# Kernel tuning notes

Hardware: AMD Instinct MI355X
Metric: run time of the kernel (lower is better)

## Reference

```python
import jax, jax.numpy as jnp
import numpy as np

DEPTH = 4
DIM = 1024
HEADS = 16
DIM_HEAD = 64
INNER = HEADS * DIM_HEAD  # 1024
MLP = 4096
CTX = 768
SCALE = DIM_HEAD ** -0.5
EPS = 1e-5


def setup_inputs() -> dict:
    key = jax.random.key(0)
    ks = jax.random.split(key, 12)
    def rn(k, shape, s=0.02):
        return jax.random.normal(k, shape, jnp.float32) * s
    return {
        "x": jax.random.normal(ks[0], (2, 2048, DIM), jnp.float32),
        "context": jax.random.normal(ks[1], (2, 1024, CTX), jnp.float32),
        "ln1_g": jnp.ones((DEPTH, DIM), jnp.float32),
        "ln1_b": jnp.zeros((DEPTH, DIM), jnp.float32),
        "w_qkv": rn(ks[2], (DEPTH, DIM, 3 * INNER)),
        "w_sa_o": rn(ks[3], (DEPTH, INNER, DIM)),
        "b_sa_o": jnp.zeros((DEPTH, DIM), jnp.float32),
        "ln2_g": jnp.ones((DEPTH, DIM), jnp.float32),
        "ln2_b": jnp.zeros((DEPTH, DIM), jnp.float32),
        "w_q": rn(ks[4], (DEPTH, DIM, INNER)),
        "w_kv": rn(ks[5], (DEPTH, CTX, 2 * INNER)),
        "w_ca_o": rn(ks[6], (DEPTH, INNER, DIM)),
        "b_ca_o": jnp.zeros((DEPTH, DIM), jnp.float32),
        "ln3_g": jnp.ones((DEPTH, DIM), jnp.float32),
        "ln3_b": jnp.zeros((DEPTH, DIM), jnp.float32),
        "w_ff1": rn(ks[7], (DEPTH, DIM, MLP)),
        "b_ff1": jnp.zeros((DEPTH, MLP), jnp.float32),
        "w_ff2": rn(ks[8], (DEPTH, MLP, DIM)),
        "b_ff2": jnp.zeros((DEPTH, DIM), jnp.float32),
    }


def _ln(x, g, b):
    mu = jnp.mean(x, axis=-1, keepdims=True)
    var = jnp.mean(jnp.square(x - mu), axis=-1, keepdims=True)
    return (x - mu) * jax.lax.rsqrt(var + EPS) * g + b


def _heads(t):
    # [b, n, h*d] -> [b, h, n, d]
    b, n, _ = t.shape
    return t.reshape(b, n, HEADS, DIM_HEAD).transpose(0, 2, 1, 3)


def _mha(q, k, v):
    # q,k,v: [b, h, n, d]; naive matmul-softmax-matmul, same math as the torch code
    attn = jax.nn.softmax(jnp.einsum('bhqd,bhkd->bhqk', q, k) * SCALE, axis=-1)
    out = jnp.einsum('bhqk,bhkd->bhqd', attn, v)
    b, h, n, d = out.shape
    return out.transpose(0, 2, 1, 3).reshape(b, n, h * d)


def reference(x, context, ln1_g, ln1_b, w_qkv, w_sa_o, b_sa_o,
              ln2_g, ln2_b, w_q, w_kv, w_ca_o, b_ca_o,
              ln3_g, ln3_b, w_ff1, b_ff1, w_ff2, b_ff2):
    for i in range(DEPTH):
        # self-attention
        h = _ln(x, ln1_g[i], ln1_b[i])
        qkv = h @ w_qkv[i]
        q, k, v = jnp.split(qkv, 3, axis=-1)
        sa = _mha(_heads(q), _heads(k), _heads(v)) @ w_sa_o[i] + b_sa_o[i]
        x = sa + x
        # cross-attention
        h = _ln(x, ln2_g[i], ln2_b[i])
        q = h @ w_q[i]
        kv = context @ w_kv[i]
        k, v = jnp.split(kv, 2, axis=-1)
        ca = _mha(_heads(q), _heads(k), _heads(v)) @ w_ca_o[i] + b_ca_o[i]
        x = ca + x
        # feed-forward (exact GELU, matching torch nn.GELU default)
        h = _ln(x, ln3_g[i], ln3_b[i])
        ff = jax.nn.gelu(h @ w_ff1[i] + b_ff1[i], approximate=False) @ w_ff2[i] + b_ff2[i]
        x = ff + x
    return x
```

## Files before the change

kernel.cpp:

```cpp
#include <hip/hip_runtime.h>
#include <hip/hip_bf16.h>
#include <math.h>

typedef __bf16 bf16_t;
typedef __bf16 bf16x8 __attribute__((ext_vector_type(8)));
typedef __bf16 bf16x4 __attribute__((ext_vector_type(4)));
typedef float f32x4 __attribute__((ext_vector_type(4)));
typedef unsigned short u16;
typedef unsigned int u32;
typedef u16 u16x8 __attribute__((ext_vector_type(8)));

#define NDEPTH 4
#define DIM 1024
#define NHEADS 16
#define MLP_DIM 4096
#define CTXD 768
#define NTOK 4096
#define NCTX 2048
#define ATT_SCALE 0.125f

__device__ inline void gload_lds16(const void* g, void* l) {
  __builtin_amdgcn_global_load_lds(
      (const __attribute__((address_space(1))) void*)g,
      (__attribute__((address_space(3))) void*)l, 16, 0, 0);
}

__device__ inline u32 packbf2(float a, float b) {
  union { bf16_t h[2]; u32 w; } u;
  u.h[0] = (bf16_t)a; u.h[1] = (bf16_t)b;
  return u.w;
}

template<int EPI>
__global__ __launch_bounds__(512) void gemm_bf16(
    const bf16_t* __restrict__ A, const bf16_t* __restrict__ Bt,
    const float* __restrict__ bias, const float* __restrict__ res,
    void* __restrict__ outp, int M, int N, int K)
{
  __shared__ alignas(16) bf16_t As[3][128 * 32];
  __shared__ alignas(16) bf16_t Bs[3][128 * 32];
  const int tid = threadIdx.x, lane = tid & 63, wave = tid >> 6;
  const int bx = blockIdx.x, by = blockIdx.y;
  const int wr = wave >> 2, wc = wave & 3;
  const int l15 = lane & 15, l4 = lane >> 4;

  const bf16_t* Ag = A + (size_t)by * 128 * K;
  const bf16_t* Bg = Bt + (size_t)bx * 128 * K;

  f32x4 acc[4][2] = {};

  const int srow = tid >> 2, soff = (tid & 3) * 8;
  auto stage = [&](int buf, int k0) {
    gload_lds16(Ag + (size_t)srow * K + k0 + soff, &As[buf][(size_t)tid * 8]);
    gload_lds16(Bg + (size_t)srow * K + k0 + soff, &Bs[buf][(size_t)tid * 8]);
  };

  const int nk = K >> 5;
  stage(0, 0);
  stage(1, 32);
  asm volatile("s_waitcnt vmcnt(2)" ::: "memory");
  __builtin_amdgcn_s_barrier();
  __builtin_amdgcn_sched_barrier(0);

  for (int t = 0; t < nk; ++t) {
    const int cur = t % 3;
    if (t + 2 < nk) stage((t + 2) % 3, (t + 2) << 5);

    bf16x8 af[4], bfr[2];
#pragma unroll
    for (int mi = 0; mi < 4; ++mi)
      af[mi] = *(const bf16x8*)&As[cur][(wr * 64 + mi * 16 + l15) * 32 + l4 * 8];
#pragma unroll
    for (int ni = 0; ni < 2; ++ni)
      bfr[ni] = *(const bf16x8*)&Bs[cur][(wc * 32 + ni * 16 + l15) * 32 + l4 * 8];
#pragma unroll
    for (int mi = 0; mi < 4; ++mi)
#pragma unroll
      for (int ni = 0; ni < 2; ++ni)
        acc[mi][ni] = __builtin_amdgcn_mfma_f32_16x16x32_bf16(af[mi], bfr[ni], acc[mi][ni], 0, 0, 0);

    if (t + 2 < nk) {
      asm volatile("s_waitcnt vmcnt(2)" ::: "memory");
    } else if (t + 1 < nk) {
      asm volatile("s_waitcnt vmcnt(0)" ::: "memory");
    } else {
      break;
    }
    __builtin_amdgcn_s_barrier();
    __builtin_amdgcn_sched_barrier(0);
  }

  const int r0 = by * 128 + wr * 64, c0 = bx * 128 + wc * 32;
#pragma unroll
  for (int ni = 0; ni < 2; ++ni) {
    int col = c0 + ni * 16 + l15;
    float bv = (EPI == 0) ? 0.f : bias[col];
#pragma unroll
    for (int mi = 0; mi < 4; ++mi) {
#pragma unroll
      for (int r = 0; r < 4; ++r) {
        int row = r0 + mi * 16 + l4 * 4 + r;
        float v = acc[mi][ni][r] + bv;
        size_t idx = (size_t)row * N + col;
        if (EPI == 3) {
          ((float*)outp)[idx] = v + res[idx];
        } else if (EPI == 2) {
          float gv = 0.5f * v * (1.f + erff(v * 0.70710678118f));
          ((bf16_t*)outp)[idx] = (bf16_t)gv;
        } else {
          ((bf16_t*)outp)[idx] = (bf16_t)v;
        }
      }
    }
  }
}

__global__ __launch_bounds__(512) void attn_fwd(
    const bf16_t* __restrict__ Q, int qs,
    const bf16_t* __restrict__ K, const bf16_t* __restrict__ V, int kvs,
    bf16_t* __restrict__ O, int os, int nq, int nk)
{
  __shared__ bf16_t Ks[2][64][72];
  __shared__ bf16_t Vt[2][64][72];

  const int tid = threadIdx.x, lane = tid & 63, wv = tid >> 6;
  const int l15 = lane & 15, l4 = lane >> 4;
  const int h = blockIdx.y, bz = blockIdx.z;
  const size_t qrow0 = (size_t)bz * nq + (size_t)blockIdx.x * 128;
  const bf16_t* Qb = Q + (qrow0 + wv * 16) * qs + h * 64;
  const bf16_t* Kb = K + (size_t)bz * nk * kvs + h * 64;
  const bf16_t* Vb = V + (size_t)bz * nk * kvs + h * 64;
  bf16_t* Ob = O + (qrow0 + wv * 16) * os + h * 64;

  bf16x8 qa[2];
#pragma unroll
  for (int ks = 0; ks < 2; ++ks)
    qa[ks] = *(const bf16x8*)(Qb + (size_t)l15 * qs + ks * 32 + l4 * 8);

  const int krow = tid >> 3, kcol = (tid & 7) * 8;

  u16x8 kreg, vreg;
  auto load_tile = [&](int kt) {
    kreg = *(const u16x8*)(Kb + (size_t)(kt * 64 + krow) * kvs + kcol);
    u16x8 t;
#pragma unroll
    for (int i = 0; i < 8; ++i)
      t[i] = *(const u16*)(Vb + (size_t)(kt * 64 + wv * 8 + i) * kvs + lane);
    vreg = t;
  };
  auto store_tile = [&](int buf) {
    *(u16x8*)&Ks[buf][krow][kcol] = kreg;
    *(u16x8*)&Vt[buf][lane][wv * 8] = vreg;
  };

  float m_run = -1e30f, l_run = 0.f;
  f32x4 acc[4] = {};

  const int ntiles = nk >> 6;
  load_tile(0);
  store_tile(0);
  __syncthreads();

  for (int kt = 0; kt < ntiles; ++kt) {
    const int cur = kt & 1;
    const bool pre = (kt + 1 < ntiles);
    if (pre) load_tile(kt + 1);

    f32x4 s[4] = {};
#pragma unroll
    for (int ks = 0; ks < 2; ++ks)
#pragma unroll
      for (int f = 0; f < 4; ++f) {
        bf16x8 kf = *(const bf16x8*)&Ks[cur][f * 16 + l15][ks * 32 + l4 * 8];
        s[f] = __builtin_amdgcn_mfma_f32_16x16x32_bf16(kf, qa[ks], s[f], 0, 0, 0);
      }

    float smax = s[0][0];
#pragma unroll
    for (int f = 0; f < 4; ++f)
#pragma unroll
      for (int r = 0; r < 4; ++r) smax = fmaxf(smax, s[f][r]);
    smax = fmaxf(smax, __shfl_xor(smax, 16));
    smax = fmaxf(smax, __shfl_xor(smax, 32));
    smax *= ATT_SCALE;
    const float mn = fmaxf(m_run, smax);
    const float esc = __expf(m_run - mn);
    m_run = mn;

    float p[4][4], psum = 0.f;
#pragma unroll
    for (int f = 0; f < 4; ++f)
#pragma unroll
      for (int r = 0; r < 4; ++r) {
        float pv = __expf(s[f][r] * ATT_SCALE - mn);
        p[f][r] = pv;
        psum += pv;
      }
    psum += __shfl_xor(psum, 16);
    psum += __shfl_xor(psum, 32);
    l_run = l_run * esc + psum;

#pragma unroll
    for (int r = 0; r < 4; ++r) {
      float eq = __shfl(esc, (l4 << 4) + (l4 << 2) + r);
#pragma unroll
      for (int d0 = 0; d0 < 4; ++d0) acc[d0][r] *= eq;
    }

    u32 pk[4][2];
#pragma unroll
    for (int f = 0; f < 4; ++f)
#pragma unroll
      for (int hh = 0; hh < 2; ++hh)
        pk[f][hh] = packbf2(p[f][2 * hh], p[f][2 * hh + 1]);

    bf16x8 pa[2];
#pragma unroll
    for (int ks = 0; ks < 2; ++ks) {
      union { u32 w[4]; bf16x8 v; } pu;
#pragma unroll
      for (int jj = 0; jj < 4; ++jj) {
        int src = l15 + ((((l4 << 1) + (jj >> 1)) & 3) << 4);
        u32 a = (u32)__shfl((int)pk[ks * 2 + 0][jj & 1], src);
        u32 b = (u32)__shfl((int)pk[ks * 2 + 1][jj & 1], src);
        pu.w[jj] = (l4 & 2) ? b : a;
      }
      pa[ks] = pu.v;
    }

#pragma unroll
    for (int ks = 0; ks < 2; ++ks)
#pragma unroll
      for (int d0 = 0; d0 < 4; ++d0) {
        bf16x8 vb = *(const bf16x8*)&Vt[cur][d0 * 16 + l15][ks * 32 + l4 * 8];
        acc[d0] = __builtin_amdgcn_mfma_f32_16x16x32_bf16(pa[ks], vb, acc[d0], 0, 0, 0);
      }

    if (pre) store_tile(cur ^ 1);
    __syncthreads();
  }

#pragma unroll
  for (int r = 0; r < 4; ++r) {
    float lq = __shfl(l_run, (l4 << 4) + (l4 << 2) + r);
    float inv = 1.f / lq;
#pragma unroll
    for (int d0 = 0; d0 < 4; ++d0)
      Ob[(size_t)(l4 * 4 + r) * os + d0 * 16 + l15] = (bf16_t)(acc[d0][r] * inv);
  }
}

__global__ __launch_bounds__(256) void layernorm_f32_bf16(
    const float* __restrict__ x, const float* __restrict__ g, const float* __restrict__ b,
    bf16_t* __restrict__ out)
{
  const int row = blockIdx.x, tid = threadIdx.x;
  const float4 v = ((const float4*)(x + (size_t)row * 1024))[tid];
  float s = v.x + v.y + v.z + v.w;
  float s2 = v.x * v.x + v.y * v.y + v.z * v.z + v.w * v.w;
#pragma unroll
  for (int off = 32; off > 0; off >>= 1) {
    s += __shfl_down(s, off);
    s2 += __shfl_down(s2, off);
  }
  __shared__ float ps[4], ps2[4];
  const int lane = tid & 63, wave = tid >> 6;
  if (lane == 0) { ps[wave] = s; ps2[wave] = s2; }
  __syncthreads();
  s = ps[0] + ps[1] + ps[2] + ps[3];
  s2 = ps2[0] + ps2[1] + ps2[2] + ps2[3];
  const float mu = s * (1.f / 1024.f);
  const float var = s2 * (1.f / 1024.f) - mu * mu;
  const float rstd = rsqrtf(var + 1e-5f);
  const float4 gv = ((const float4*)g)[tid];
  const float4 bv = ((const float4*)b)[tid];
  bf16x4 o;
  o[0] = (bf16_t)((v.x - mu) * rstd * gv.x + bv.x);
  o[1] = (bf16_t)((v.y - mu) * rstd * gv.y + bv.y);
  o[2] = (bf16_t)((v.z - mu) * rstd * gv.z + bv.z);
  o[3] = (bf16_t)((v.w - mu) * rstd * gv.w + bv.w);
  *(bf16x4*)(out + (size_t)row * 1024 + tid * 4) = o;
}

__global__ void transpose_to_bf16(const float* __restrict__ src, bf16_t* __restrict__ dst, int K, int N)
{
  __shared__ float tile[32][33];
  const size_t loff = (size_t)blockIdx.z * K * N;
  src += loff; dst += loff;
  const int k0 = blockIdx.y * 32, n0 = blockIdx.x * 32;
  const int tx = threadIdx.x, ty = threadIdx.y;
#pragma unroll
  for (int i = ty; i < 32; i += 8)
    tile[i][tx] = src[(size_t)(k0 + i) * N + n0 + tx];
  __syncthreads();
#pragma unroll
  for (int i = ty; i < 32; i += 8)
    dst[(size_t)(n0 + i) * K + k0 + tx] = (bf16_t)tile[tx][i];
}

__global__ void f32_to_bf16(const float* __restrict__ src, bf16_t* __restrict__ dst, int n4)
{
  int i = blockIdx.x * blockDim.x + threadIdx.x;
  if (i < n4) {
    float4 v = ((const float4*)src)[i];
    bf16x4 o;
    o[0] = (bf16_t)v.x; o[1] = (bf16_t)v.y; o[2] = (bf16_t)v.z; o[3] = (bf16_t)v.w;
    ((bf16x4*)dst)[i] = o;
  }
}

__global__ void copy_f32(const float* __restrict__ src, float* __restrict__ dst, int n4)
{
  int i = blockIdx.x * blockDim.x + threadIdx.x;
  if (i < n4) ((float4*)dst)[i] = ((const float4*)src)[i];
}

extern "C" void kernel_launch(void* const* d_in, const int* in_sizes, int n_in,
                              void* d_out, int out_size, void* d_ws, size_t ws_size,
                              hipStream_t stream)
{
  const float* x      = (const float*)d_in[0];
  const float* ctx    = (const float*)d_in[1];
  const float* ln1_g  = (const float*)d_in[2];
  const float* ln1_b  = (const float*)d_in[3];
  const float* w_qkv  = (const float*)d_in[4];
  const float* w_sa_o = (const float*)d_in[5];
  const float* b_sa_o = (const float*)d_in[6];
  const float* ln2_g  = (const float*)d_in[7];
  const float* ln2_b  = (const float*)d_in[8];
  const float* w_q    = (const float*)d_in[9];
  const float* w_kv   = (const float*)d_in[10];
  const float* w_ca_o = (const float*)d_in[11];
  const float* b_ca_o = (const float*)d_in[12];
  const float* ln3_g  = (const float*)d_in[13];
  const float* ln3_b  = (const float*)d_in[14];
  const float* w_ff1  = (const float*)d_in[15];
  const float* b_ff1  = (const float*)d_in[16];
  const float* w_ff2  = (const float*)d_in[17];
  const float* b_ff2  = (const float*)d_in[18];

  char* p = (char*)d_ws;
  auto alloc = [&](size_t bytes) { char* r = p; p += (bytes + 255) & ~(size_t)255; return r; };
  bf16_t* wqkv_t = (bf16_t*)alloc((size_t)NDEPTH * 3072 * 1024 * 2);
  bf16_t* wsao_t = (bf16_t*)alloc((size_t)NDEPTH * 1024 * 1024 * 2);
  bf16_t* wq_t   = (bf16_t*)alloc((size_t)NDEPTH * 1024 * 1024 * 2);
  bf16_t* wkv_t  = (bf16_t*)alloc((size_t)NDEPTH * 2048 * 768 * 2);
  bf16_t* wcao_t = (bf16_t*)alloc((size_t)NDEPTH * 1024 * 1024 * 2);
  bf16_t* wff1_t = (bf16_t*)alloc((size_t)NDEPTH * 4096 * 1024 * 2);
  bf16_t* wff2_t = (bf16_t*)alloc((size_t)NDEPTH * 1024 * 4096 * 2);
  bf16_t* ctxb   = (bf16_t*)alloc((size_t)NCTX * CTXD * 2);
  float*  xbuf   = (float*)alloc((size_t)NTOK * DIM * 4);
  bf16_t* lnbuf  = (bf16_t*)alloc((size_t)NTOK * DIM * 2);
  bf16_t* bigbuf = (bf16_t*)alloc((size_t)NTOK * 4096 * 2);
  bf16_t* qbuf   = (bf16_t*)alloc((size_t)NTOK * DIM * 2);
  bf16_t* kvbuf  = (bf16_t*)alloc((size_t)NCTX * 2048 * 2);
  if ((size_t)(p - (char*)d_ws) > ws_size) return;

  dim3 tb(32, 8);
  transpose_to_bf16<<<dim3(3072 / 32, 1024 / 32, NDEPTH), tb, 0, stream>>>(w_qkv, wqkv_t, 1024, 3072);
  transpose_to_bf16<<<dim3(1024 / 32, 1024 / 32, NDEPTH), tb, 0, stream>>>(w_sa_o, wsao_t, 1024, 1024);
  transpose_to_bf16<<<dim3(1024 / 32, 1024 / 32, NDEPTH), tb, 0, stream>>>(w_q, wq_t, 1024, 1024);
  transpose_to_bf16<<<dim3(2048 / 32, 768 / 32, NDEPTH), tb, 0, stream>>>(w_kv, wkv_t, 768, 2048);
  transpose_to_bf16<<<dim3(1024 / 32, 1024 / 32, NDEPTH), tb, 0, stream>>>(w_ca_o, wcao_t, 1024, 1024);
  transpose_to_bf16<<<dim3(4096 / 32, 1024 / 32, NDEPTH), tb, 0, stream>>>(w_ff1, wff1_t, 1024, 4096);
  transpose_to_bf16<<<dim3(1024 / 32, 4096 / 32, NDEPTH), tb, 0, stream>>>(w_ff2, wff2_t, 4096, 1024);
  f32_to_bf16<<<(NCTX * CTXD / 4 + 255) / 256, 256, 0, stream>>>(ctx, ctxb, NCTX * CTXD / 4);
  copy_f32<<<(NTOK * DIM / 4 + 255) / 256, 256, 0, stream>>>(x, xbuf, NTOK * DIM / 4);

  for (int i = 0; i < NDEPTH; ++i) {
    layernorm_f32_bf16<<<NTOK, 256, 0, stream>>>(xbuf, ln1_g + i * DIM, ln1_b + i * DIM, lnbuf);
    gemm_bf16<0><<<dim3(3072 / 128, NTOK / 128), 512, 0, stream>>>(
        lnbuf, wqkv_t + (size_t)i * 3072 * 1024, nullptr, nullptr, bigbuf, NTOK, 3072, 1024);
    attn_fwd<<<dim3(2048 / 128, NHEADS, 2), 512, 0, stream>>>(
        bigbuf, 3072, bigbuf + 1024, bigbuf + 2048, 3072, lnbuf, 1024, 2048, 2048);
    gemm_bf16<3><<<dim3(1024 / 128, NTOK / 128), 512, 0, stream>>>(
        lnbuf, wsao_t + (size_t)i * 1024 * 1024, b_sa_o + i * DIM, xbuf, xbuf, NTOK, 1024, 1024);
    layernorm_f32_bf16<<<NTOK, 256, 0, stream>>>(xbuf, ln2_g + i * DIM, ln2_b + i * DIM, lnbuf);
    gemm_bf16<0><<<dim3(1024 / 128, NTOK / 128), 512, 0, stream>>>(
        lnbuf, wq_t + (size_t)i * 1024 * 1024, nullptr, nullptr, qbuf, NTOK, 1024, 1024);
    gemm_bf16<0><<<dim3(2048 / 128, NCTX / 128), 512, 0, stream>>>(
        ctxb, wkv_t + (size_t)i * 2048 * 768, nullptr, nullptr, kvbuf, NCTX, 2048, 768);
    attn_fwd<<<dim3(2048 / 128, NHEADS, 2), 512, 0, stream>>>(
        qbuf, 1024, kvbuf, kvbuf + 1024, 2048, lnbuf, 1024, 2048, 1024);
    gemm_bf16<3><<<dim3(1024 / 128, NTOK / 128), 512, 0, stream>>>(
        lnbuf, wcao_t + (size_t)i * 1024 * 1024, b_ca_o + i * DIM, xbuf, xbuf, NTOK, 1024, 1024);
    layernorm_f32_bf16<<<NTOK, 256, 0, stream>>>(xbuf, ln3_g + i * DIM, ln3_b + i * DIM, lnbuf);
    gemm_bf16<2><<<dim3(4096 / 128, NTOK / 128), 512, 0, stream>>>(
        lnbuf, wff1_t + (size_t)i * 4096 * 1024, b_ff1 + i * MLP_DIM, nullptr, bigbuf, NTOK, 4096, 1024);
    gemm_bf16<3><<<dim3(1024 / 128, NTOK / 128), 512, 0, stream>>>(
        bigbuf, wff2_t + (size_t)i * 1024 * 4096, b_ff2 + i * DIM, xbuf, xbuf, NTOK, 1024, 4096);
  }
  copy_f32<<<(NTOK * DIM / 4 + 255) / 256, 256, 0, stream>>>(xbuf, (float*)d_out, NTOK * DIM / 4);
}
```

Baseline: 1.864 ms.

## Add 64x64-tile GEMM for narrow projections and lazy softmax rescaling in attention

Adds a 256-thread GEMM kernel with 64x64 tiles and uses it for the N=1024 and N=2048 projections (out-projections, Q, KV, FF2). The 128-tile grid for these shapes launched only 256 blocks, which fills the CUs poorly, and the smaller tile is meant to raise the block count. Attention now rescales the running max, sum and accumulator only when the new block max exceeds the old one by more than a threshold, skipping the exp and multiplies most of the time. The costs are lower per-block operand reuse in the small GEMM and the possibility of larger exponent values before the normalisation catches up.

```diff
diff --git a/kernel.cpp b/kernel.cpp
--- a/kernel.cpp
+++ b/kernel.cpp
@@ -29,6 +29,20 @@
   union { bf16_t h[2]; u32 w; } u;
   u.h[0] = (bf16_t)a; u.h[1] = (bf16_t)b;
   return u.w;
+}
+
+template<int EPI>
+__device__ inline void epi_store(void* outp, const float* bias, const float* res,
+                                 int row, int col, int N, float v) {
+  size_t idx = (size_t)row * N + col;
+  if (EPI == 3) {
+    ((float*)outp)[idx] = v + bias[col] + res[idx];
+  } else if (EPI == 2) {
+    float vb = v + bias[col];
+    ((bf16_t*)outp)[idx] = (bf16_t)(0.5f * vb * (1.f + erff(vb * 0.70710678118f)));
+  } else {
+    ((bf16_t*)outp)[idx] = (bf16_t)v;
+  }
 }
 
 template<int EPI>
@@ -92,27 +106,83 @@
 
   const int r0 = by * 128 + wr * 64, c0 = bx * 128 + wc * 32;
 #pragma unroll
-  for (int ni = 0; ni < 2; ++ni) {
-    int col = c0 + ni * 16 + l15;
-    float bv = (EPI == 0) ? 0.f : bias[col];
-#pragma unroll
-    for (int mi = 0; mi < 4; ++mi) {
-#pragma unroll
-      for (int r = 0; r < 4; ++r) {
-        int row = r0 + mi * 16 + l4 * 4 + r;
-        float v = acc[mi][ni][r] + bv;
-        size_t idx = (size_t)row * N + col;
-        if (EPI == 3) {
-          ((float*)outp)[idx] = v + res[idx];
-        } else if (EPI == 2) {
-          float gv = 0.5f * v * (1.f + erff(v * 0.70710678118f));
-          ((bf16_t*)outp)[idx] = (bf16_t)gv;
-        } else {
-          ((bf16_t*)outp)[idx] = (bf16_t)v;
-        }
-      }
+  for (int ni = 0; ni < 2; ++ni)
+#pragma unroll
+    for (int mi = 0; mi < 4; ++mi)
+#pragma unroll
+      for (int r = 0; r < 4; ++r)
+        epi_store<EPI>(outp, bias, res, r0 + mi * 16 + l4 * 4 + r,
+                       c0 + ni * 16 + l15, N, acc[mi][ni][r]);
+}
+
+template<int EPI>
+__global__ __launch_bounds__(256) void gemm64_bf16(
+    const bf16_t* __restrict__ A, const bf16_t* __restrict__ Bt,
+    const float* __restrict__ bias, const float* __restrict__ res,
+    void* __restrict__ outp, int M, int N, int K)
+{
+  __shared__ alignas(16) bf16_t As[3][64 * 32];
+  __shared__ alignas(16) bf16_t Bs[3][64 * 32];
+  const int tid = threadIdx.x, lane = tid & 63, wave = tid >> 6;
+  const int bx = blockIdx.x, by = blockIdx.y;
+  const int wr = wave >> 1, wc = wave & 1;
+  const int l15 = lane & 15, l4 = lane >> 4;
+
+  const bf16_t* Ag = A + (size_t)by * 64 * K;
+  const bf16_t* Bg = Bt + (size_t)bx * 64 * K;
+
+  f32x4 acc[2][2] = {};
+
+  const int srow = tid >> 2, soff = (tid & 3) * 8;
+  auto stage = [&](int buf, int k0) {
+    gload_lds16(Ag + (size_t)srow * K + k0 + soff, &As[buf][(size_t)tid * 8]);
+    gload_lds16(Bg + (size_t)srow * K + k0 + soff, &Bs[buf][(size_t)tid * 8]);
+  };
+
+  const int nk = K >> 5;
+  stage(0, 0);
+  stage(1, 32);
+  asm volatile("s_waitcnt vmcnt(2)" ::: "memory");
+  __builtin_amdgcn_s_barrier();
+  __builtin_amdgcn_sched_barrier(0);
+
+  for (int t = 0; t < nk; ++t) {
+    const int cur = t % 3;
+    if (t + 2 < nk) stage((t + 2) % 3, (t + 2) << 5);
+
+    bf16x8 af[2], bfr[2];
+#pragma unroll
+    for (int mi = 0; mi < 2; ++mi)
+      af[mi] = *(const bf16x8*)&As[cur][(wr * 32 + mi * 16 + l15) * 32 + l4 * 8];
+#pragma unroll
+    for (int ni = 0; ni < 2; ++ni)
+      bfr[ni] = *(const bf16x8*)&Bs[cur][(wc * 32 + ni * 16 + l15) * 32 + l4 * 8];
+#pragma unroll
+    for (int mi = 0; mi < 2; ++mi)
+#pragma unroll
+      for (int ni = 0; ni < 2; ++ni)
+        acc[mi][ni] = __builtin_amdgcn_mfma_f32_16x16x32_bf16(af[mi], bfr[ni], acc[mi][ni], 0, 0, 0);
+
+    if (t + 2 < nk) {
+      asm volatile("s_waitcnt vmcnt(2)" ::: "memory");
+    } else if (t + 1 < nk) {
+      asm volatile("s_waitcnt vmcnt(0)" ::: "memory");
+    } else {
+      break;
     }
-  }
+    __builtin_amdgcn_s_barrier();
+    __builtin_amdgcn_sched_barrier(0);
+  }
+
+  const int r0 = by * 64 + wr * 32, c0 = bx * 64 + wc * 32;
+#pragma unroll
+  for (int ni = 0; ni < 2; ++ni)
+#pragma unroll
+    for (int mi = 0; mi < 2; ++mi)
+#pragma unroll
+      for (int r = 0; r < 4; ++r)
+        epi_store<EPI>(outp, bias, res, r0 + mi * 16 + l4 * 4 + r,
+                       c0 + ni * 16 + l15, N, acc[mi][ni][r]);
 }
 
 __global__ __launch_bounds__(512) void attn_fwd(
@@ -183,29 +253,32 @@
     smax = fmaxf(smax, __shfl_xor(smax, 16));
     smax = fmaxf(smax, __shfl_xor(smax, 32));
     smax *= ATT_SCALE;
-    const float mn = fmaxf(m_run, smax);
-    const float esc = __expf(m_run - mn);
-    m_run = mn;
+
+    if (!__all(smax <= m_run + 8.f)) {
+      const float mn = fmaxf(m_run, smax);
+      const float esc = __expf(m_run - mn);
+      m_run = mn;
+      l_run *= esc;
+#pragma unroll
+      for (int r = 0; r < 4; ++r) {
+        float eq = __shfl(esc, (l4 << 4) + (l4 << 2) + r);
+#pragma unroll
+        for (int d0 = 0; d0 < 4; ++d0) acc[d0][r] *= eq;
+      }
+    }
 
     float p[4][4], psum = 0.f;
 #pragma unroll
     for (int f = 0; f < 4; ++f)
 #pragma unroll
       for (int r = 0; r < 4; ++r) {
-        float pv = __expf(s[f][r] * ATT_SCALE - mn);
+        float pv = __expf(s[f][r] * ATT_SCALE - m_run);
         p[f][r] = pv;
         psum += pv;
       }
     psum += __shfl_xor(psum, 16);
     psum += __shfl_xor(psum, 32);
-    l_run = l_run * esc + psum;
-
-#pragma unroll
-    for (int r = 0; r < 4; ++r) {
-      float eq = __shfl(esc, (l4 << 4) + (l4 << 2) + r);
-#pragma unroll
-      for (int d0 = 0; d0 < 4; ++d0) acc[d0][r] *= eq;
-    }
+    l_run += psum;
 
     u32 pk[4][2];
 #pragma unroll
@@ -373,21 +446,21 @@
         lnbuf, wqkv_t + (size_t)i * 3072 * 1024, nullptr, nullptr, bigbuf, NTOK, 3072, 1024);
     attn_fwd<<<dim3(2048 / 128, NHEADS, 2), 512, 0, stream>>>(
         bigbuf, 3072, bigbuf + 1024, bigbuf + 2048, 3072, lnbuf, 1024, 2048, 2048);
-    gemm_bf16<3><<<dim3(1024 / 128, NTOK / 128), 512, 0, stream>>>(
+    gemm64_bf16<3><<<dim3(1024 / 64, NTOK / 64), 256, 0, stream>>>(
         lnbuf, wsao_t + (size_t)i * 1024 * 1024, b_sa_o + i * DIM, xbuf, xbuf, NTOK, 1024, 1024);
     layernorm_f32_bf16<<<NTOK, 256, 0, stream>>>(xbuf, ln2_g + i * DIM, ln2_b + i * DIM, lnbuf);
-    gemm_bf16<0><<<dim3(1024 / 128, NTOK / 128), 512, 0, stream>>>(
+    gemm64_bf16<0><<<dim3(1024 / 64, NTOK / 64), 256, 0, stream>>>(
         lnbuf, wq_t + (size_t)i * 1024 * 1024, nullptr, nullptr, qbuf, NTOK, 1024, 1024);
-    gemm_bf16<0><<<dim3(2048 / 128, NCTX / 128), 512, 0, stream>>>(
+    gemm64_bf16<0><<<dim3(2048 / 64, NCTX / 64), 256, 0, stream>>>(
         ctxb, wkv_t + (size_t)i * 2048 * 768, nullptr, nullptr, kvbuf, NCTX, 2048, 768);
     attn_fwd<<<dim3(2048 / 128, NHEADS, 2), 512, 0, stream>>>(
         qbuf, 1024, kvbuf, kvbuf + 1024, 2048, lnbuf, 1024, 2048, 1024);
-    gemm_bf16<3><<<dim3(1024 / 128, NTOK / 128), 512, 0, stream>>>(
+    gemm64_bf16<3><<<dim3(1024 / 64, NTOK / 64), 256, 0, stream>>>(
         lnbuf, wcao_t + (size_t)i * 1024 * 1024, b_ca_o + i * DIM, xbuf, xbuf, NTOK, 1024, 1024);
     layernorm_f32_bf16<<<NTOK, 256, 0, stream>>>(xbuf, ln3_g + i * DIM, ln3_b + i * DIM, lnbuf);
     gemm_bf16<2><<<dim3(4096 / 128, NTOK / 128), 512, 0, stream>>>(
         lnbuf, wff1_t + (size_t)i * 4096 * 1024, b_ff1 + i * MLP_DIM, nullptr, bigbuf, NTOK, 4096, 1024);
-    gemm_bf16<3><<<dim3(1024 / 128, NTOK / 128), 512, 0, stream>>>(
+    gemm64_bf16<3><<<dim3(1024 / 64, NTOK / 64), 256, 0, stream>>>(
         bigbuf, wff2_t + (size_t)i * 1024 * 4096, b_ff2 + i * DIM, xbuf, xbuf, NTOK, 1024, 4096);
   }
   copy_f32<<<(NTOK * DIM / 4 + 255) / 256, 256, 0, stream>>>(xbuf, (float*)d_out, NTOK * DIM / 4);
```

Result: faster. 1.803 ms (-3.3%).
